# Kernel tuning notes

Measured on AMD Instinct MI355X. Metric: run time of the kernel, lower is better.

## Reference

```python
import jax, jax.numpy as jnp
import numpy as np

V, H, L, NH, I, P, B, S = 30000, 768, 12, 12, 3072, 512, 8, 512
D = H // NH  # 64, size_per_head
STD = 0.02
LN_EPS = 1e-3  # Keras LayerNormalization default epsilon


def setup_inputs() -> dict:
    key = jax.random.key(0)
    ks = jax.random.split(key, 16)
    n = lambda k, shape: (jax.random.normal(k, shape, jnp.float32) * STD)
    return {
        "input_ids": jax.random.randint(ks[0], (B, S), 0, V, dtype=jnp.int32),
        "input_mask": jnp.ones((B, S), jnp.int32),
        "token_type_ids": jnp.zeros((B, S), jnp.int32),
        "tok_emb": n(ks[1], (V, H)),
        "pos_emb": n(ks[2], (P, H)),
        "type_emb": n(ks[3], (2, H)),
        "emb_ln_g": jnp.ones((H,), jnp.float32),
        "emb_ln_b": jnp.zeros((H,), jnp.float32),
        "Wq": n(ks[4], (L, H, H)), "bq": jnp.zeros((L, H), jnp.float32),
        "Wk": n(ks[5], (L, H, H)), "bk": jnp.zeros((L, H), jnp.float32),
        "Wv": n(ks[6], (L, H, H)), "bv": jnp.zeros((L, H), jnp.float32),
        "Wo": n(ks[7], (L, H, H)), "bo": jnp.zeros((L, H), jnp.float32),
        "ln1_g": jnp.ones((L, H), jnp.float32), "ln1_b": jnp.zeros((L, H), jnp.float32),
        "Wi": n(ks[8], (L, H, I)), "bi": jnp.zeros((L, I), jnp.float32),
        "Wd": n(ks[9], (L, I, H)), "bd": jnp.zeros((L, H), jnp.float32),
        "ln2_g": jnp.ones((L, H), jnp.float32), "ln2_b": jnp.zeros((L, H), jnp.float32),
    }


def layer_norm(x, g, b):
    mu = jnp.mean(x, axis=-1, keepdims=True)
    var = jnp.mean(jnp.square(x - mu), axis=-1, keepdims=True)
    return (x - mu) * jax.lax.rsqrt(var + LN_EPS) * g + b


def bert_forward(input_ids, input_mask, token_type_ids,
                 tok_emb, pos_emb, type_emb, emb_ln_g, emb_ln_b,
                 Wq, bq, Wk, bk, Wv, bv, Wo, bo, ln1_g, ln1_b,
                 Wi, bi, Wd, bd, ln2_g, ln2_b):
    b, s = input_ids.shape
    # embeddings: token + segment + position, then layernorm (dropout off at inference)
    x = tok_emb[input_ids] + type_emb[token_type_ids] + pos_emb[:s][None, :, :]
    x = layer_norm(x, emb_ln_g, emb_ln_b)

    # additive attention bias from 2D mask: (1 - m) * -10000, broadcast over heads/queries
    mask_bias = (1.0 - input_mask.astype(jnp.float32))[:, None, None, :] * -10000.0  # [b,1,1,s]
    scale = 1.0 / np.sqrt(float(D))

    def block(h, p):
        wq, bq_, wk, bk_, wv, bv_, wo, bo_, g1, b1, wi, bi_, wd, bd_, g2, b2 = p
        # QKV projections, split heads -> [b, nh, s, d]
        split = lambda t: t.reshape(b, s, NH, D).transpose(0, 2, 1, 3)
        q = split(h @ wq + bq_)
        k = split(h @ wk + bk_)
        v = split(h @ wv + bv_)
        scores = jnp.einsum('bhqd,bhkd->bhqk', q, k) * scale + mask_bias
        probs = jax.nn.softmax(scores, axis=-1)
        o = jnp.einsum('bhqk,bhkd->bhqd', probs, v)
        o = o.transpose(0, 2, 1, 3).reshape(b, s, H)
        attn = layer_norm(o @ wo + bo_ + h, g1, b1)
        ffn = jax.nn.gelu(attn @ wi + bi_, approximate=False) @ wd + bd_
        out = layer_norm(ffn + attn, g2, b2)
        return out, None

    params = (Wq, bq, Wk, bk, Wv, bv, Wo, bo, ln1_g, ln1_b, Wi, bi, Wd, bd, ln2_g, ln2_b)
    x, _ = jax.lax.scan(block, x, params)
    return x


def reference(input_ids, input_mask, token_type_ids,
              tok_emb, pos_emb, type_emb, emb_ln_g, emb_ln_b,
              Wq, bq, Wk, bk, Wv, bv, Wo, bo, ln1_g, ln1_b,
              Wi, bi, Wd, bd, ln2_g, ln2_b):
    return bert_forward(input_ids, input_mask, token_type_ids,
                        tok_emb, pos_emb, type_emb, emb_ln_g, emb_ln_b,
                        Wq, bq, Wk, bk, Wv, bv, Wo, bo, ln1_g, ln1_b,
                        Wi, bi, Wd, bd, ln2_g, ln2_b)
```

## Files before the change

kernel.cpp:

```cpp
#include <hip/hip_runtime.h>
#include <math.h>

#define NHEADS 12
#define DHEAD  64
#define SEQL   512
#define HID    768
#define IMID   3072
#define NTOK   4096
#define NLAY   12

typedef __attribute__((ext_vector_type(8))) short short8;
typedef __attribute__((ext_vector_type(4))) float f32x4;

__device__ __forceinline__ short f2b(float f) {
    union { float f; unsigned u; } v; v.f = f;
    unsigned r = (v.u + 0x7fffu + ((v.u >> 16) & 1u)) >> 16;
    return (short)r;
}
__device__ __forceinline__ float b2f(short h) {
    union { unsigned u; float f; } v; v.u = ((unsigned)(unsigned short)h) << 16;
    return v.f;
}
__device__ __forceinline__ void mfma16(f32x4& c, short8 a, short8 b) {
    asm volatile("v_mfma_f32_16x16x32_bf16 %0, %1, %2, %0" : "+v"(c) : "v"(a), "v"(b));
}
__device__ __forceinline__ void accfence() {
    __builtin_amdgcn_sched_barrier(0);
    asm volatile("s_nop 7\ns_nop 7\ns_nop 7\ns_nop 7");
    __builtin_amdgcn_sched_barrier(0);
}
__device__ __forceinline__ void gload_lds16(const void* g, void* l) {
    __builtin_amdgcn_global_load_lds(
        (const __attribute__((address_space(1))) unsigned int*)g,
        (__attribute__((address_space(3))) unsigned int*)l, 16, 0, 0);
}

__global__ __launch_bounds__(256) void wconv_k(
    const float* __restrict__ src, short* __restrict__ dst,
    int K, int N, size_t dlsz, int rowStart, float scale)
{
    __shared__ short t[64][72];
    src += (size_t)blockIdx.z * K * N;
    dst += (size_t)blockIdx.z * dlsz;
    const int k0 = blockIdx.x * 64, n0 = blockIdx.y * 64;
    const int kr = threadIdx.x >> 2, q = threadIdx.x & 3;
    const float* s = src + (size_t)(k0 + kr) * N + n0 + q * 16;
#pragma unroll
    for (int j = 0; j < 16; j += 4) {
        float4 v = *reinterpret_cast<const float4*>(s + j);
        t[q * 16 + j + 0][kr] = f2b(v.x * scale);
        t[q * 16 + j + 1][kr] = f2b(v.y * scale);
        t[q * 16 + j + 2][kr] = f2b(v.z * scale);
        t[q * 16 + j + 3][kr] = f2b(v.w * scale);
    }
    __syncthreads();
    const int r = threadIdx.x >> 2;
    short* d = dst + (size_t)(rowStart + n0 + r) * K + k0 + q * 16;
    *reinterpret_cast<short8*>(d)     = *reinterpret_cast<short8*>(&t[r][q * 16]);
    *reinterpret_cast<short8*>(d + 8) = *reinterpret_cast<short8*>(&t[r][q * 16 + 8]);
}

__global__ __launch_bounds__(256) void bpack_k(
    const float* __restrict__ bq, const float* __restrict__ bk,
    const float* __restrict__ bv, float* __restrict__ dst)
{
    int i = blockIdx.x * 256 + threadIdx.x;
    if (i >= NLAY * 2304) return;
    int l = i / 2304, c = i % 2304;
    float v = c < 768 ? 0.125f * bq[l * 768 + c]
            : c < 1536 ? bk[l * 768 + c - 768] : bv[l * 768 + c - 1536];
    dst[i] = v;
}

__global__ __launch_bounds__(256) void embed_ln_k(
    const int* __restrict__ ids, const int* __restrict__ tti,
    const float* __restrict__ tokE, const float* __restrict__ posE,
    const float* __restrict__ typE, const float* __restrict__ g,
    const float* __restrict__ bb, float* __restrict__ x, short* __restrict__ xb)
{
    __shared__ float red[8];
    const int t = blockIdx.x, s = t & (SEQL - 1);
    const int id = ids[t], ty = tti[t];
    float v[3], sum = 0.f, sq = 0.f;
#pragma unroll
    for (int i = 0; i < 3; ++i) {
        const int c = threadIdx.x + 256 * i;
        float e = tokE[(size_t)id * HID + c] + typE[(size_t)ty * HID + c]
                + posE[(size_t)s * HID + c];
        v[i] = e; sum += e; sq += e * e;
    }
#pragma unroll
    for (int d = 1; d < 64; d <<= 1) { sum += __shfl_xor(sum, d); sq += __shfl_xor(sq, d); }
    const int lane = threadIdx.x & 63, w = threadIdx.x >> 6;
    if (lane == 0) { red[w] = sum; red[4 + w] = sq; }
    __syncthreads();
    sum = red[0] + red[1] + red[2] + red[3];
    sq  = red[4] + red[5] + red[6] + red[7];
    const float mu = sum * (1.0f / 768.0f);
    const float var = sq * (1.0f / 768.0f) - mu * mu;
    const float rstd = rsqrtf(var + 1e-3f);
#pragma unroll
    for (int i = 0; i < 3; ++i) {
        const int c = threadIdx.x + 256 * i;
        float yv = (v[i] - mu) * rstd * g[c] + bb[c];
        x[(size_t)t * HID + c] = yv;
        xb[(size_t)t * HID + c] = f2b(yv);
    }
}

__global__ __launch_bounds__(256) void add_ln_k(
    const float* __restrict__ y, const float* __restrict__ res,
    const float* __restrict__ g, const float* __restrict__ bb,
    float* __restrict__ xout, short* __restrict__ bout, float* __restrict__ fout)
{
    __shared__ float red[8];
    const int t = blockIdx.x;
    float v[3], sum = 0.f, sq = 0.f;
#pragma unroll
    for (int i = 0; i < 3; ++i) {
        const int c = threadIdx.x + 256 * i;
        float e = y[(size_t)t * HID + c] + res[(size_t)t * HID + c];
        v[i] = e; sum += e; sq += e * e;
    }
#pragma unroll
    for (int d = 1; d < 64; d <<= 1) { sum += __shfl_xor(sum, d); sq += __shfl_xor(sq, d); }
    const int lane = threadIdx.x & 63, w = threadIdx.x >> 6;
    if (lane == 0) { red[w] = sum; red[4 + w] = sq; }
    __syncthreads();
    sum = red[0] + red[1] + red[2] + red[3];
    sq  = red[4] + red[5] + red[6] + red[7];
    const float mu = sum * (1.0f / 768.0f);
    const float var = sq * (1.0f / 768.0f) - mu * mu;
    const float rstd = rsqrtf(var + 1e-3f);
#pragma unroll
    for (int i = 0; i < 3; ++i) {
        const int c = threadIdx.x + 256 * i;
        float yv = (v[i] - mu) * rstd * g[c] + bb[c];
        xout[(size_t)t * HID + c] = yv;
        bout[(size_t)t * HID + c] = f2b(yv);
        if (fout) fout[(size_t)t * HID + c] = yv;
    }
}

__global__ __launch_bounds__(256) void add_ln_red_k(
    const float* __restrict__ p0, const float* __restrict__ p1,
    const float* __restrict__ res, const float* __restrict__ g,
    const float* __restrict__ bb, float* __restrict__ xout,
    short* __restrict__ bout, float* __restrict__ fout)
{
    __shared__ float red[8];
    const int t = blockIdx.x;
    float v[3], sum = 0.f, sq = 0.f;
#pragma unroll
    for (int i = 0; i < 3; ++i) {
        const int c = threadIdx.x + 256 * i;
        const size_t o = (size_t)t * HID + c;
        float e = p0[o] + p1[o] + res[o];
        v[i] = e; sum += e; sq += e * e;
    }
#pragma unroll
    for (int d = 1; d < 64; d <<= 1) { sum += __shfl_xor(sum, d); sq += __shfl_xor(sq, d); }
    const int lane = threadIdx.x & 63, w = threadIdx.x >> 6;
    if (lane == 0) { red[w] = sum; red[4 + w] = sq; }
    __syncthreads();
    sum = red[0] + red[1] + red[2] + red[3];
    sq  = red[4] + red[5] + red[6] + red[7];
    const float mu = sum * (1.0f / 768.0f);
    const float var = sq * (1.0f / 768.0f) - mu * mu;
    const float rstd = rsqrtf(var + 1e-3f);
#pragma unroll
    for (int i = 0; i < 3; ++i) {
        const int c = threadIdx.x + 256 * i;
        float yv = (v[i] - mu) * rstd * g[c] + bb[c];
        xout[(size_t)t * HID + c] = yv;
        bout[(size_t)t * HID + c] = f2b(yv);
        if (fout) fout[(size_t)t * HID + c] = yv;
    }
}

__global__ __launch_bounds__(256) void add_ln_red3_k(
    const float* __restrict__ p0, const float* __restrict__ p1,
    const float* __restrict__ p2, const float* __restrict__ res,
    const float* __restrict__ g, const float* __restrict__ bb,
    float* __restrict__ xout, short* __restrict__ bout, float* __restrict__ fout)
{
    __shared__ float red[8];
    const int t = blockIdx.x;
    float v[3], sum = 0.f, sq = 0.f;
#pragma unroll
    for (int i = 0; i < 3; ++i) {
        const int c = threadIdx.x + 256 * i;
        const size_t o = (size_t)t * HID + c;
        float e = p0[o] + p1[o] + p2[o] + res[o];
        v[i] = e; sum += e; sq += e * e;
    }
#pragma unroll
    for (int d = 1; d < 64; d <<= 1) { sum += __shfl_xor(sum, d); sq += __shfl_xor(sq, d); }
    const int lane = threadIdx.x & 63, w = threadIdx.x >> 6;
    if (lane == 0) { red[w] = sum; red[4 + w] = sq; }
    __syncthreads();
    sum = red[0] + red[1] + red[2] + red[3];
    sq  = red[4] + red[5] + red[6] + red[7];
    const float mu = sum * (1.0f / 768.0f);
    const float var = sq * (1.0f / 768.0f) - mu * mu;
    const float rstd = rsqrtf(var + 1e-3f);
#pragma unroll
    for (int i = 0; i < 3; ++i) {
        const int c = threadIdx.x + 256 * i;
        float yv = (v[i] - mu) * rstd * g[c] + bb[c];
        xout[(size_t)t * HID + c] = yv;
        bout[(size_t)t * HID + c] = f2b(yv);
        if (fout) fout[(size_t)t * HID + c] = yv;
    }
}

template<int EPI>
__global__ __launch_bounds__(256) void gemm3_k(
    const short* __restrict__ A, const short* __restrict__ Wt,
    const float* __restrict__ bias, void* __restrict__ Out, int K, int N, int kChunk,
    void* __restrict__ Out2, void* __restrict__ Out3)
{
    __shared__ short sA[3][128 * 32];
    __shared__ short sB[3][128 * 32];
    const int tid = threadIdx.x;
    const int lane = tid & 63, wave = tid >> 6;
    const int wm = wave >> 1, wn = wave & 1;
    const int rl = lane & 15, hi = lane >> 4;

    const int nb = gridDim.x, bid = blockIdx.x;
    const int id = (bid & 7) * (nb >> 3) + (bid >> 3);
    const int m0 = (id & 31) * 128, n0 = (id >> 5) * 128;
    const int kBeg = blockIdx.y * kChunk;

    f32x4 acc[4][4];
#pragma unroll
    for (int i = 0; i < 4; ++i)
#pragma unroll
        for (int j = 0; j < 4; ++j)
            acc[i][j] = (f32x4){0.f, 0.f, 0.f, 0.f};

    auto stage = [&](int buf, int k0) {
#pragma unroll
        for (int i = 0; i < 2; ++i) {
            const int gb = wave * 128 + i * 64;
            const int gid = gb + lane;
            const int row = gid >> 2, sg = gid & 3;
            const int ksw = (sg ^ ((row >> 1) & 3)) << 3;
            gload_lds16(&A[(size_t)(m0 + row) * K + k0 + ksw], &sA[buf][gb * 8]);
            gload_lds16(&Wt[(size_t)(n0 + row) * K + k0 + ksw], &sB[buf][gb * 8]);
        }
    };

    const int nIter = kChunk >> 5;
    stage(0, kBeg);
    if (nIter > 1) stage(1, kBeg + 32);
    for (int t = 0; t < nIter; ++t) {
        const int cur = t % 3;
        if (t + 2 < nIter) {
            stage((t + 2) % 3, kBeg + (t + 2) * 32);
            __builtin_amdgcn_sched_barrier(0);
            asm volatile("s_waitcnt vmcnt(8)" ::: "memory");
        } else if (t + 1 < nIter) {
            __builtin_amdgcn_sched_barrier(0);
            asm volatile("s_waitcnt vmcnt(4)" ::: "memory");
        } else {
            __builtin_amdgcn_sched_barrier(0);
            asm volatile("s_waitcnt vmcnt(0)" ::: "memory");
        }
        __builtin_amdgcn_s_barrier();
        __builtin_amdgcn_sched_barrier(0);

        short8 af[4], bfr[4];
#pragma unroll
        for (int f = 0; f < 4; ++f) {
            const int ra = wm * 64 + f * 16 + rl;
            const int rb = wn * 64 + f * 16 + rl;
            af[f]  = *reinterpret_cast<const short8*>(&sA[cur][ra * 32 + ((hi ^ ((ra >> 1) & 3)) << 3)]);
            bfr[f] = *reinterpret_cast<const short8*>(&sB[cur][rb * 32 + ((hi ^ ((rb >> 1) & 3)) << 3)]);
        }
#pragma unroll
        for (int i = 0; i < 4; ++i)
#pragma unroll
            for (int j = 0; j < 4; ++j)
                mfma16(acc[i][j], af[i], bfr[j]);

        asm volatile("s_waitcnt lgkmcnt(0)" ::: "memory");
        __builtin_amdgcn_sched_barrier(0);
        __builtin_amdgcn_s_barrier();
    }
    accfence();
    float* skDst = nullptr;
    if (EPI == 6)
        skDst = blockIdx.y == 0 ? (float*)Out : (blockIdx.y == 1 ? (float*)Out2 : (float*)Out3);
#pragma unroll
    for (int j = 0; j < 4; ++j) {
        const int col = n0 + wn * 64 + j * 16 + rl;
        const float bv = (EPI == 6 && blockIdx.y != 0) ? 0.f : bias[col];
#pragma unroll
        for (int i = 0; i < 4; ++i) {
#pragma unroll
            for (int e = 0; e < 4; ++e) {
                const int row = m0 + wm * 64 + i * 16 + hi * 4 + e;
                float v = acc[i][j][e] + bv;
                if (EPI == 0) {
                    ((float*)Out)[(size_t)row * N + col] = v;
                } else if (EPI == 1) {
                    float gl = 0.5f * v * (1.0f + erff(v * 0.70710678118f));
                    ((short*)Out)[(size_t)row * N + col] = f2b(gl);
                } else if (EPI == 6) {
                    skDst[(size_t)row * N + col] = v;
                } else {
                    const int sec = col >= 1536 ? 2 : (col >= 768 ? 1 : 0);
                    const int cc = col - sec * 768;
                    const int b = row >> 9, s = row & 511, nh = cc >> 6, d = cc & 63;
                    short* o = (short*)Out + (size_t)sec * 3145728;
                    if (sec == 2)
                        o[(((size_t)(b * NHEADS + nh) * DHEAD + d) << 9) + s] = f2b(v);
                    else
                        o[(((size_t)(b * NHEADS + nh) * SEQL + s) << 6) + d] = f2b(v);
                }
            }
        }
    }
}

template<int EPI>
__global__ __launch_bounds__(256) void gemm_k(
    const short* __restrict__ A, const float* __restrict__ W,
    const float* __restrict__ bias, void* __restrict__ Out, int K, int N)
{
    __shared__ short sA[128 * 40];
    __shared__ short sB[128 * 40];
    const int tid = threadIdx.x;
    const int lane = tid & 63, wave = tid >> 6;
    const int wm = wave >> 1, wn = wave & 1;
    const int m0 = blockIdx.x * 128, n0 = blockIdx.y * 128;
    const int rl = lane & 15, hi = lane >> 4;

    f32x4 acc[4][4];
#pragma unroll
    for (int i = 0; i < 4; ++i)
#pragma unroll
        for (int j = 0; j < 4; ++j)
            acc[i][j] = (f32x4){0.f, 0.f, 0.f, 0.f};

    const int arow = tid >> 2, ac8 = (tid & 3) << 3;
    const int bk0 = tid >> 5, bn4 = (tid & 31) << 2;

    for (int k0 = 0; k0 < K; k0 += 32) {
#pragma unroll
        for (int i = 0; i < 2; ++i) {
            int row = i * 64 + arow;
            short8 v = *reinterpret_cast<const short8*>(&A[(size_t)(m0 + row) * K + k0 + ac8]);
            *reinterpret_cast<short8*>(&sA[row * 40 + ac8]) = v;
        }
#pragma unroll
        for (int p = 0; p < 4; ++p) {
            int kk = p * 8 + bk0;
            float4 w4 = *reinterpret_cast<const float4*>(&W[(size_t)(k0 + kk) * N + n0 + bn4]);
            sB[(bn4 + 0) * 40 + kk] = f2b(w4.x);
            sB[(bn4 + 1) * 40 + kk] = f2b(w4.y);
            sB[(bn4 + 2) * 40 + kk] = f2b(w4.z);
            sB[(bn4 + 3) * 40 + kk] = f2b(w4.w);
        }
        __syncthreads();
        short8 af[4], bfr[4];
#pragma unroll
        for (int f = 0; f < 4; ++f) {
            af[f]  = *reinterpret_cast<const short8*>(&sA[(wm * 64 + f * 16 + rl) * 40 + hi * 8]);
            bfr[f] = *reinterpret_cast<const short8*>(&sB[(wn * 64 + f * 16 + rl) * 40 + hi * 8]);
        }
#pragma unroll
        for (int i = 0; i < 4; ++i)
#pragma unroll
            for (int j = 0; j < 4; ++j)
                mfma16(acc[i][j], af[i], bfr[j]);
        __syncthreads();
    }
    accfence();
#pragma unroll
    for (int j = 0; j < 4; ++j) {
        const int col = n0 + wn * 64 + j * 16 + rl;
        const float bv = bias[col];
#pragma unroll
        for (int i = 0; i < 4; ++i) {
#pragma unroll
            for (int e = 0; e < 4; ++e) {
                const int row = m0 + wm * 64 + i * 16 + hi * 4 + e;
                float v = acc[i][j][e] + bv;
                if (EPI == 0) {
                    ((float*)Out)[(size_t)row * N + col] = v;
                } else if (EPI == 1) {
                    float gl = 0.5f * v * (1.0f + erff(v * 0.70710678118f));
                    ((short*)Out)[(size_t)row * N + col] = f2b(gl);
                } else {
                    const int b = row >> 9, s = row & 511, nh = col >> 6, d = col & 63;
                    if (EPI == 2)
                        ((short*)Out)[(((size_t)(b * NHEADS + nh) * SEQL + s) << 6) + d] = f2b(v * 0.125f);
                    else if (EPI == 3)
                        ((short*)Out)[(((size_t)(b * NHEADS + nh) * SEQL + s) << 6) + d] = f2b(v);
                    else
                        ((short*)Out)[(((size_t)(b * NHEADS + nh) * DHEAD + d) << 9) + s] = f2b(v);
                }
            }
        }
    }
}

__global__ __launch_bounds__(256) void attn_k(
    const short* __restrict__ q, const short* __restrict__ k,
    const short* __restrict__ vt, const int* __restrict__ mask,
    short* __restrict__ ctx)
{
    __shared__ short sQ[32 * 72];
    __shared__ short sP[32 * 520];
    __shared__ float wreds[128];

    const int blk = blockIdx.x;
    const int qb = blk & 15, bh = blk >> 4;
    const int b = bh / NHEADS, h = bh % NHEADS;
    const int tid = threadIdx.x, lane = tid & 63, wave = tid >> 6;
    const int rl = lane & 15, hi = lane >> 4;
    const short* __restrict__ qh = q + (size_t)bh * SEQL * DHEAD;
    const short* __restrict__ kh = k + (size_t)bh * SEQL * DHEAD;
    const short* __restrict__ vh = vt + (size_t)bh * DHEAD * SEQL;

    {
        int row = tid >> 3, c8 = (tid & 7) << 3;
        *reinterpret_cast<short8*>(&sQ[row * 72 + c8]) =
            *reinterpret_cast<const short8*>(&qh[(size_t)(qb * 32 + row) * DHEAD + c8]);
    }

    float mb[8];
#pragma unroll
    for (int fn = 0; fn < 8; ++fn) {
        int n = wave * 128 + fn * 16 + rl;
        mb[fn] = -10000.0f * (1.0f - (float)mask[b * SEQL + n]);
    }
    __syncthreads();

    f32x4 sacc[2][8];
#pragma unroll
    for (int mf = 0; mf < 2; ++mf)
#pragma unroll
        for (int fn = 0; fn < 8; ++fn)
            sacc[mf][fn] = (f32x4){0.f, 0.f, 0.f, 0.f};
    __builtin_amdgcn_s_setprio(1);
#pragma unroll
    for (int ks = 0; ks < 2; ++ks) {
        short8 a0 = *reinterpret_cast<const short8*>(&sQ[rl * 72 + ks * 32 + hi * 8]);
        short8 a1 = *reinterpret_cast<const short8*>(&sQ[(16 + rl) * 72 + ks * 32 + hi * 8]);
#pragma unroll
        for (int fn = 0; fn < 8; ++fn) {
            int n = wave * 128 + fn * 16 + rl;
            short8 bk = *reinterpret_cast<const short8*>(&kh[(size_t)n * DHEAD + ks * 32 + hi * 8]);
            mfma16(sacc[0][fn], a0, bk);
            mfma16(sacc[1][fn], a1, bk);
        }
    }
    __builtin_amdgcn_s_setprio(0);
    accfence();

    float rsum[2][4] = {{0.f, 0.f, 0.f, 0.f}, {0.f, 0.f, 0.f, 0.f}};
#pragma unroll
    for (int mf = 0; mf < 2; ++mf)
#pragma unroll
        for (int fn = 0; fn < 8; ++fn)
#pragma unroll
            for (int e = 0; e < 4; ++e) {
                float p = __expf(sacc[mf][fn][e] + mb[fn]);
                rsum[mf][e] += p;
                sP[(mf * 16 + hi * 4 + e) * 520 + wave * 128 + fn * 16 + rl] = f2b(p);
            }
#pragma unroll
    for (int d = 1; d < 16; d <<= 1)
#pragma unroll
        for (int mf = 0; mf < 2; ++mf)
#pragma unroll
            for (int e = 0; e < 4; ++e)
                rsum[mf][e] += __shfl_xor(rsum[mf][e], d);
    if (rl == 0) {
#pragma unroll
        for (int mf = 0; mf < 2; ++mf)
#pragma unroll
            for (int e = 0; e < 4; ++e)
                wreds[wave * 32 + mf * 16 + hi * 4 + e] = rsum[mf][e];
    }
    __syncthreads();
    float rsf[2][4];
#pragma unroll
    for (int mf = 0; mf < 2; ++mf)
#pragma unroll
        for (int e = 0; e < 4; ++e) {
            const int row = mf * 16 + hi * 4 + e;
            rsf[mf][e] = wreds[row] + wreds[32 + row] + wreds[64 + row] + wreds[96 + row];
        }

    f32x4 oacc[2];
    oacc[0] = (f32x4){0.f, 0.f, 0.f, 0.f};
    oacc[1] = (f32x4){0.f, 0.f, 0.f, 0.f};
    __builtin_amdgcn_s_setprio(1);
#pragma unroll
    for (int ks = 0; ks < 16; ++ks) {
        short8 p0 = *reinterpret_cast<const short8*>(&sP[rl * 520 + ks * 32 + hi * 8]);
        short8 p1 = *reinterpret_cast<const short8*>(&sP[(16 + rl) * 520 + ks * 32 + hi * 8]);
        short8 bv = *reinterpret_cast<const short8*>(&vh[(size_t)(wave * 16 + rl) * SEQL + ks * 32 + hi * 8]);
        mfma16(oacc[0], p0, bv);
        mfma16(oacc[1], p1, bv);
    }
    __builtin_amdgcn_s_setprio(0);
    accfence();
#pragma unroll
    for (int mf = 0; mf < 2; ++mf) {
#pragma unroll
        for (int e = 0; e < 4; ++e) {
            const int row = mf * 16 + hi * 4 + e;
            const int s = qb * 32 + row;
            const int d = wave * 16 + rl;
            float o = oacc[mf][e] * __builtin_amdgcn_rcpf(rsf[mf][e]);
            ctx[((size_t)(b * SEQL + s)) * HID + h * DHEAD + d] = f2b(o);
        }
    }
}

extern "C" void kernel_launch(void* const* d_in, const int* in_sizes, int n_in,
                              void* d_out, int out_size, void* d_ws, size_t ws_size,
                              hipStream_t stream)
{
    const int*   ids  = (const int*)d_in[0];
    const int*   msk  = (const int*)d_in[1];
    const int*   tti  = (const int*)d_in[2];
    const float* tokE = (const float*)d_in[3];
    const float* posE = (const float*)d_in[4];
    const float* typE = (const float*)d_in[5];
    const float* elg  = (const float*)d_in[6];
    const float* elb  = (const float*)d_in[7];
    const float* Wq   = (const float*)d_in[8];  const float* bq = (const float*)d_in[9];
    const float* Wk   = (const float*)d_in[10]; const float* bk = (const float*)d_in[11];
    const float* Wv   = (const float*)d_in[12]; const float* bv = (const float*)d_in[13];
    const float* Wo   = (const float*)d_in[14]; const float* bo = (const float*)d_in[15];
    const float* g1   = (const float*)d_in[16]; const float* b1 = (const float*)d_in[17];
    const float* Wi   = (const float*)d_in[18]; const float* bi = (const float*)d_in[19];
    const float* Wd   = (const float*)d_in[20]; const float* bd = (const float*)d_in[21];
    const float* g2   = (const float*)d_in[22]; const float* b2 = (const float*)d_in[23];

    if (ws_size < 81788928u) return;
    char* ws = (char*)d_ws;
    float* x   = (float*)(ws);
    float* y   = (float*)(ws + 12582912);
    short* xb  = (short*)(ws + 25165824);
    short* qq  = (short*)(ws + 31457280);
    short* kk_ = (short*)(ws + 37748736);
    short* vv  = (short*)(ws + 44040192);
    short* ctx = (short*)(ws + 50331648);
    short* f1  = (short*)(ws + 56623104);
    float* pp  = (float*)(ws + 31457280);
    float* pp2 = (float*)(ws + 44040192);

    embed_ln_k<<<NTOK, 256, 0, stream>>>(ids, tti, tokE, posE, typE, elg, elb, x, xb);

    const bool fast = ws_size >= 251768832u;
    if (fast) {
        short* qkvT = (short*)(ws + 81788928);
        short* woT  = (short*)(ws + 124256256);
        short* wiT  = (short*)(ws + 138412032);
        short* wdT  = (short*)(ws + 195035136);
        float* bqkv = (float*)(ws + 251658240);

        wconv_k<<<dim3(12, 12, NLAY), 256, 0, stream>>>(Wq, qkvT, 768, 768, 2304 * 768, 0, 0.125f);
        wconv_k<<<dim3(12, 12, NLAY), 256, 0, stream>>>(Wk, qkvT, 768, 768, 2304 * 768, 768, 1.0f);
        wconv_k<<<dim3(12, 12, NLAY), 256, 0, stream>>>(Wv, qkvT, 768, 768, 2304 * 768, 1536, 1.0f);
        wconv_k<<<dim3(12, 12, NLAY), 256, 0, stream>>>(Wo, woT, 768, 768, 768 * 768, 0, 1.0f);
        wconv_k<<<dim3(12, 48, NLAY), 256, 0, stream>>>(Wi, wiT, 768, 3072, 3072 * 768, 0, 1.0f);
        wconv_k<<<dim3(48, 12, NLAY), 256, 0, stream>>>(Wd, wdT, 3072, 768, 768 * 3072, 0, 1.0f);
        bpack_k<<<108, 256, 0, stream>>>(bq, bk, bv, bqkv);

        for (int l = 0; l < NLAY; ++l) {
            const size_t oH = (size_t)l * HID, oI = (size_t)l * IMID;
            gemm3_k<5><<<dim3(576, 1), 256, 0, stream>>>(xb, qkvT + (size_t)l * 2304 * 768,
                                                         bqkv + (size_t)l * 2304, qq, 768, 2304, 768,
                                                         nullptr, nullptr);
            attn_k<<<1536, 256, 0, stream>>>(qq, kk_, vv, msk, ctx);
            gemm3_k<6><<<dim3(192, 2), 256, 0, stream>>>(ctx, woT + (size_t)l * 768 * 768,
                                                         bo + oH, y, 768, 768, 384, pp, nullptr);
            add_ln_red_k<<<NTOK, 256, 0, stream>>>(y, pp, x, g1 + oH, b1 + oH, x, xb, nullptr);
            gemm3_k<1><<<dim3(768, 1), 256, 0, stream>>>(xb, wiT + (size_t)l * 3072 * 768,
                                                         bi + oI, f1, 768, 3072, 768,
                                                         nullptr, nullptr);
            gemm3_k<6><<<dim3(192, 3), 256, 0, stream>>>(f1, wdT + (size_t)l * 768 * 3072,
                                                         bd + oH, y, 3072, 768, 1024, pp, pp2);
            add_ln_red3_k<<<NTOK, 256, 0, stream>>>(y, pp, pp2, x, g2 + oH, b2 + oH, x, xb,
                                                    (l == NLAY - 1) ? (float*)d_out : nullptr);
        }
    } else {
        const dim3 g6(32, 6), g24(32, 24);
        for (int l = 0; l < NLAY; ++l) {
            const size_t oHH = (size_t)l * HID * HID, oH = (size_t)l * HID;
            const size_t oHI = (size_t)l * HID * IMID, oI = (size_t)l * IMID;
            gemm_k<2><<<g6, 256, 0, stream>>>(xb, Wq + oHH, bq + oH, qq, HID, HID);
            gemm_k<3><<<g6, 256, 0, stream>>>(xb, Wk + oHH, bk + oH, kk_, HID, HID);
            gemm_k<4><<<g6, 256, 0, stream>>>(xb, Wv + oHH, bv + oH, vv, HID, HID);
            attn_k<<<1536, 256, 0, stream>>>(qq, kk_, vv, msk, ctx);
            gemm_k<0><<<g6, 256, 0, stream>>>(ctx, Wo + oHH, bo + oH, y, HID, HID);
            add_ln_k<<<NTOK, 256, 0, stream>>>(y, x, g1 + oH, b1 + oH, x, xb, nullptr);
            gemm_k<1><<<g24, 256, 0, stream>>>(xb, Wi + oHI, bi + oI, f1, HID, IMID);
            gemm_k<0><<<g6, 256, 0, stream>>>(f1, Wd + oHI, bd + oH, y, IMID, HID);
            add_ln_k<<<NTOK, 256, 0, stream>>>(y, x, g2 + oH, b2 + oH, x, xb,
                                               (l == NLAY - 1) ? (float*)d_out : nullptr);
        }
    }
}
```

Measured before the change: 2.485 ms.

## Write V linearly from QKV GEMM, transpose in separate kernel; swizzle attention blocks

```diff
diff --git a/kernel.cpp b/kernel.cpp
--- a/kernel.cpp
+++ b/kernel.cpp
@@ -70,6 +70,27 @@
     float v = c < 768 ? 0.125f * bq[l * 768 + c]
             : c < 1536 ? bk[l * 768 + c - 768] : bv[l * 768 + c - 1536];
     dst[i] = v;
+}
+
+__global__ __launch_bounds__(256) void vtr_k(
+    const short* __restrict__ src, short* __restrict__ dst)
+{
+    __shared__ short t[64][80];
+    const int sT = blockIdx.x;
+    const int nh = blockIdx.y;
+    const int r = threadIdx.x >> 2, q = threadIdx.x & 3;
+    const short* s = src + (size_t)(sT * 64 + r) * HID + nh * 64 + q * 16;
+    short8 v0 = *reinterpret_cast<const short8*>(s);
+    short8 v1 = *reinterpret_cast<const short8*>(s + 8);
+#pragma unroll
+    for (int j = 0; j < 8; ++j) t[q * 16 + j][r] = v0[j];
+#pragma unroll
+    for (int j = 0; j < 8; ++j) t[q * 16 + 8 + j][r] = v1[j];
+    __syncthreads();
+    const int b = sT >> 3, s0 = (sT & 7) * 64;
+    short* d = dst + (((size_t)(b * NHEADS + nh) * DHEAD + r) << 9) + s0 + q * 16;
+    *reinterpret_cast<short8*>(d)     = *reinterpret_cast<short8*>(&t[r][q * 16]);
+    *reinterpret_cast<short8*>(d + 8) = *reinterpret_cast<short8*>(&t[r][q * 16 + 8]);
 }
 
 __global__ __launch_bounds__(256) void embed_ln_k(
@@ -310,14 +331,15 @@
                 } else if (EPI == 6) {
                     skDst[(size_t)row * N + col] = v;
                 } else {
-                    const int sec = col >= 1536 ? 2 : (col >= 768 ? 1 : 0);
-                    const int cc = col - sec * 768;
-                    const int b = row >> 9, s = row & 511, nh = cc >> 6, d = cc & 63;
-                    short* o = (short*)Out + (size_t)sec * 3145728;
-                    if (sec == 2)
-                        o[(((size_t)(b * NHEADS + nh) * DHEAD + d) << 9) + s] = f2b(v);
-                    else
+                    if (col >= 1536) {
+                        ((short*)Out3)[(size_t)row * HID + (col - 1536)] = f2b(v);
+                    } else {
+                        const int sec = col >= 768 ? 1 : 0;
+                        const int cc = col - sec * 768;
+                        const int b = row >> 9, s = row & 511, nh = cc >> 6, d = cc & 63;
+                        short* o = (short*)Out + (size_t)sec * 3145728;
                         o[(((size_t)(b * NHEADS + nh) * SEQL + s) << 6) + d] = f2b(v);
+                    }
                 }
             }
         }
@@ -416,7 +438,8 @@
     __shared__ short sP[32 * 520];
     __shared__ float wreds[128];
 
-    const int blk = blockIdx.x;
+    const int orig = blockIdx.x;
+    const int blk = (orig & 7) * (gridDim.x >> 3) + (orig >> 3);
     const int qb = blk & 15, bh = blk >> 4;
     const int b = bh / NHEADS, h = bh % NHEADS;
     const int tid = threadIdx.x, lane = tid & 63, wave = tid >> 6;
@@ -566,6 +589,7 @@
         short* wiT  = (short*)(ws + 138412032);
         short* wdT  = (short*)(ws + 195035136);
         float* bqkv = (float*)(ws + 251658240);
+        short* vlin = f1;
 
         wconv_k<<<dim3(12, 12, NLAY), 256, 0, stream>>>(Wq, qkvT, 768, 768, 2304 * 768, 0, 0.125f);
         wconv_k<<<dim3(12, 12, NLAY), 256, 0, stream>>>(Wk, qkvT, 768, 768, 2304 * 768, 768, 1.0f);
@@ -579,7 +603,8 @@
             const size_t oH = (size_t)l * HID, oI = (size_t)l * IMID;
             gemm3_k<5><<<dim3(576, 1), 256, 0, stream>>>(xb, qkvT + (size_t)l * 2304 * 768,
                                                          bqkv + (size_t)l * 2304, qq, 768, 2304, 768,
-                                                         nullptr, nullptr);
+                                                         nullptr, vlin);
+            vtr_k<<<dim3(64, 12), 256, 0, stream>>>(vlin, vv);
             attn_k<<<1536, 256, 0, stream>>>(qq, kk_, vv, msk, ctx);
             gemm3_k<6><<<dim3(192, 2), 256, 0, stream>>>(ctx, woT + (size_t)l * 768 * 768,
                                                          bo + oH, y, 768, 768, 384, pp, nullptr);
```

Result: faster. 2.292 ms (-7.8%).
